# Kernel optimization log

Hardware: AMD Instinct MI355X
Metric: run time of the kernel (lower is better)

Reference implementation:

```python
import jax, jax.numpy as jnp
import numpy as np

N_NODES = 8192
N_EDGES = 65536
MUL = 16          # multiplicity of 0e and 1o irreps
NB = 16           # num_radial_basis
HID = 16          # num_radial_dimension
MAX_RADIUS = 5.0
SQRT3 = float(np.sqrt(3.0))


def soft_unit_step(x):
    # e3nn.math.soft_unit_step: exp(-1/x) for x>0 else 0 (grad-safe where)
    safe = jnp.where(x > 0, x, 1.0)
    return jnp.where(x > 0, jnp.exp(-1.0 / safe), 0.0)


def setup_inputs() -> dict:
    key = jax.random.key(0)
    ks = jax.random.split(key, 12)
    f_in = jax.random.normal(ks[0], (N_NODES, 4 * MUL), jnp.float32)
    edge_vec = jax.random.normal(ks[1], (N_EDGES, 3), jnp.float32) * 1.5
    edge_src = jax.random.randint(ks[2], (N_EDGES,), 0, N_NODES)
    edge_dst = jax.random.randint(ks[3], (N_EDGES,), 0, N_NODES)
    Wq0 = jax.random.normal(ks[4], (MUL, MUL), jnp.float32)
    Wq1 = jax.random.normal(ks[5], (MUL, MUL), jnp.float32)
    Wk1 = jax.random.normal(ks[6], (NB, HID), jnp.float32)
    Wk2 = jax.random.normal(ks[7], (HID, 4 * MUL * MUL), jnp.float32)
    Wv1 = jax.random.normal(ks[8], (NB, HID), jnp.float32)
    Wv2 = jax.random.normal(ks[9], (HID, 4 * MUL * MUL), jnp.float32)
    Wd0 = jax.random.normal(ks[10], (MUL, MUL), jnp.float32)
    Wd1 = jax.random.normal(ks[11], (MUL, MUL), jnp.float32)
    return dict(f_in=f_in, edge_vec=edge_vec, edge_src=edge_src, edge_dst=edge_dst,
                Wq0=Wq0, Wq1=Wq1, Wk1=Wk1, Wk2=Wk2, Wv1=Wv1, Wv2=Wv2, Wd0=Wd0, Wd1=Wd1)


def _forward(f_in, edge_vec, edge_src, edge_dst,
             Wq0, Wq1, Wk1, Wk2, Wv1, Wv2, Wd0, Wd1):
    f0 = f_in[:, :MUL]                         # [N, MUL]    0e scalars
    f1 = f_in[:, MUL:].reshape(-1, MUL, 3)     # [N, MUL, 3] 1o vectors

    r = jnp.linalg.norm(edge_vec, axis=1)      # [E]
    u = edge_vec / r[:, None]
    sh1 = SQRT3 * u                            # Y_1, component norm (|Y1|^2 = 3); Y_0 = 1

    # soft_one_hot_linspace, basis='smooth_finite', cutoff=True, * sqrt(NB)
    values = jnp.linspace(0.0, MAX_RADIUS, NB + 2)
    step = values[1] - values[0]
    diff = (r[:, None] - values[1:-1]) / step
    C = 1.14136 * float(np.exp(2.0))
    rb = (C * soft_unit_step(diff + 1.0) * soft_unit_step(1.0 - diff)) * np.sqrt(NB)

    edge_cut = soft_unit_step(10.0 * (1.0 - r / MAX_RADIUS))  # [E]

    def mlp(x, W1, W2):  # e3nn FullyConnectedNet with fan-in normalization
        h = jax.nn.silu(x @ (W1 / np.sqrt(NB)))
        return h @ (W2 / np.sqrt(HID))

    wk = mlp(rb, Wk1, Wk2).reshape(-1, 4, MUL, MUL)  # per-edge TP weights
    wv = mlp(rb, Wv1, Wv2).reshape(-1, 4, MUL, MUL)

    # h_q: per-irrep linear
    q0 = f0 @ Wq0 / np.sqrt(MUL)
    q1 = jnp.einsum('nic,io->noc', f1, Wq1) / np.sqrt(MUL)

    x0 = f0[edge_src]   # [E, MUL]
    x1 = f1[edge_src]   # [E, MUL, 3]

    def fctp(w):
        # FullyConnectedTensorProduct (16x0e+16x1o) x (0e+1o) -> (16x0e+16x1o)
        # 4 paths: 0x0->0, 1x1->0 (dot/sqrt3), 0x1->1, 1x0->1
        a = 1.0 / np.sqrt(2 * MUL)
        o0 = jnp.einsum('eij,ei->ej', w[:, 0], x0) \
           + jnp.einsum('eij,eic,ec->ej', w[:, 1], x1, sh1) / SQRT3
        o1 = jnp.einsum('eij,ei,ec->ejc', w[:, 2], x0, sh1) \
           + jnp.einsum('eij,eic->ejc', w[:, 3], x1)
        return o0 * a, o1 * a

    k0, k1 = fctp(wk)
    v0, v1 = fctp(wv)

    # dot_product: FCTP(query, key) -> 0e
    ad = 1.0 / np.sqrt(2.0 * MUL * MUL)
    dot = ad * (jnp.einsum('ij,ei,ej->e', Wd0, q0[edge_dst], k0)
                + jnp.einsum('ij,eic,ejc->e', Wd1, q1[edge_dst], k1) / SQRT3)

    exp = edge_cut * jnp.exp(dot)                                   # [E]
    z = jax.ops.segment_sum(exp, edge_dst, num_segments=N_NODES)    # [N]
    z = jnp.where(z == 0.0, 1.0, z)
    alpha = exp / z[edge_dst]
    # alpha.relu().sqrt() with grad-safe sqrt at 0
    s = jnp.where(alpha > 0, jnp.sqrt(jnp.where(alpha > 0, alpha, 1.0)), 0.0)

    f_out0 = jax.ops.segment_sum(s[:, None] * v0, edge_dst, num_segments=N_NODES)
    f_out1 = jax.ops.segment_sum(s[:, None, None] * v1, edge_dst, num_segments=N_NODES)
    return jnp.concatenate([f_out0, f_out1.reshape(-1, MUL * 3)], axis=-1)  # [N, 64]


def reference(f_in, edge_vec, edge_src, edge_dst,
              Wq0, Wq1, Wk1, Wk2, Wv1, Wv2, Wd0, Wd1):
    return _forward(f_in, edge_vec, edge_src, edge_dst,
                    Wq0, Wq1, Wk1, Wk2, Wv1, Wv2, Wd0, Wd1)
```

## Files before the change

### kernel.cpp

```cpp
#include <hip/hip_runtime.h>
#include <hip/hip_bf16.h>

#define N_NODES 8192
#define N_EDGES 65536

#define Z_OFF    0
#define CNT_OFF  8192
#define RP_OFF   16384
#define WF_OFF   24832
#define QD0_OFF  41216
#define QD1_OFF  172288
#define EXP_OFF  565504
#define EIDX_OFF 631040
#define V_OFF    696576

typedef _Float16 half8 __attribute__((ext_vector_type(8)));
typedef float f32x4 __attribute__((ext_vector_type(4)));

__device__ __forceinline__ float sus_f(float x) { return x > 0.f ? expf(-1.f / x) : 0.f; }
__device__ __forceinline__ float silu_f(float x) { return x / (1.f + expf(-x)); }

__device__ __forceinline__ half8 vmul(half8 v, _Float16 s) {
    half8 r;
#pragma unroll
    for (int d = 0; d < 8; ++d) r[d] = v[d] * s;
    return r;
}

__global__ __launch_bounds__(256) void k_prep(
    const float* __restrict__ f_in,
    const float* __restrict__ Wq0, const float* __restrict__ Wq1,
    const float* __restrict__ Wd0, const float* __restrict__ Wd1,
    const float* __restrict__ Wk2, const float* __restrict__ Wv2,
    const int* __restrict__ edst,
    half8* __restrict__ wfrag, float* __restrict__ qd0, float* __restrict__ qd1,
    int* __restrict__ cnt) {
    __shared__ float f0s[16][16];
    __shared__ float f1s[16][48];
    __shared__ float t0s[16][16];
    __shared__ float t1s[16][48];
    const int blk = blockIdx.x;
    const int tid = threadIdx.x;

    if (blk < 16) {
        int g = blk * 256 + tid;
        int lane = g & 63, t = (g >> 6) & 7, b = (g >> 9) & 3, kv = g >> 11;
        const float* src = kv ? Wv2 : Wk2;
        int n = lane & 15, quad = lane >> 4;
        const float SC = 0.044194173824159216f;
        half8 out;
#pragma unroll
        for (int d = 0; d < 8; ++d) {
            int k = t * 32 + quad * 8 + d;
            int i = k & 15, h = k >> 4;
            out[d] = (_Float16)(src[h * 1024 + b * 256 + i * 16 + n] * SC);
        }
        wfrag[g] = out;
        return;
    }
    if (blk >= 528) {
        int base = (blk - 528) * 256 + tid;
#pragma unroll
        for (int k = 0; k < 4; ++k) atomicAdd(cnt + edst[base + k * 16384], 1);
        return;
    }
    const int j = tid & 15, ln = tid >> 4;
    const int n = (blk - 16) * 16 + ln;
    f0s[ln][j]         = f_in[n * 64 + j];
    f1s[ln][j * 3 + 0] = f_in[n * 64 + 16 + j * 3 + 0];
    f1s[ln][j * 3 + 1] = f_in[n * 64 + 16 + j * 3 + 1];
    f1s[ln][j * 3 + 2] = f_in[n * 64 + 16 + j * 3 + 2];
    __syncthreads();
    float t0 = 0.f, ta = 0.f, tb = 0.f, tc = 0.f;
#pragma unroll
    for (int p = 0; p < 16; ++p) {
        float wq0 = Wq0[p * 16 + j];
        float wq1 = Wq1[p * 16 + j];
        t0 += f0s[ln][p] * wq0;
        ta += f1s[ln][p * 3 + 0] * wq1;
        tb += f1s[ln][p * 3 + 1] * wq1;
        tc += f1s[ln][p * 3 + 2] * wq1;
    }
    t0s[ln][j] = t0;
    t1s[ln][j * 3 + 0] = ta; t1s[ln][j * 3 + 1] = tb; t1s[ln][j * 3 + 2] = tc;
    __syncthreads();
    float q0a = 0.f, qa = 0.f, qb = 0.f, qc = 0.f;
#pragma unroll
    for (int i = 0; i < 16; ++i) {
        float wd0 = Wd0[i * 16 + j];
        float wd1 = Wd1[i * 16 + j];
        q0a += t0s[ln][i] * wd0;
        qa  += t1s[ln][i * 3 + 0] * wd1;
        qb  += t1s[ln][i * 3 + 1] * wd1;
        qc  += t1s[ln][i * 3 + 2] * wd1;
    }
    const float S0 = 0.011048543456f;
    const float S1 = 0.0063788674817f;
    qd0[n * 16 + j] = q0a * S0;
    qd1[0 * 131072 + n * 16 + j] = qa * S1;
    qd1[1 * 131072 + n * 16 + j] = qb * S1;
    qd1[2 * 131072 + n * 16 + j] = qc * S1;
}

__global__ __launch_bounds__(1024) void k_scan(int* __restrict__ cnt, int* __restrict__ rowptr) {
    __shared__ int part[1024];
    const int t = threadIdx.x;
    const int base = t * 8;
    int v[8]; int s = 0;
#pragma unroll
    for (int i = 0; i < 8; ++i) { v[i] = cnt[base + i]; s += v[i]; }
    part[t] = s;
    __syncthreads();
    for (int off = 1; off < 1024; off <<= 1) {
        int x = (t >= off) ? part[t - off] : 0;
        __syncthreads();
        part[t] += x;
        __syncthreads();
    }
    int run = part[t] - s;
#pragma unroll
    for (int i = 0; i < 8; ++i) { rowptr[base + i] = run; cnt[base + i] = run; run += v[i]; }
    if (t == 1023) rowptr[8192] = run;
}

__global__ void k_scidx(const int* __restrict__ edst, int* __restrict__ cnt,
                        int* __restrict__ eidx) {
    int e = blockIdx.x * blockDim.x + threadIdx.x;
    int slot = atomicAdd(cnt + edst[e], 1);
    eidx[slot] = e;
}

__global__ __launch_bounds__(256) void k_edge(
    const float* __restrict__ f_in, const float* __restrict__ evec,
    const int* __restrict__ esrc, const int* __restrict__ edst,
    const float* __restrict__ Wk1, const float* __restrict__ Wv1,
    const half8* __restrict__ wfrag,
    const float* __restrict__ qd0, const float* __restrict__ qd1,
    float* __restrict__ zbuf, float* __restrict__ expbuf, float* __restrict__ vbuf) {
    __shared__ __align__(16) _Float16 s_x0h[64][24];
    __shared__ __align__(16) _Float16 s_xsh[64][24];
    __shared__ __align__(16) _Float16 s_x1h[3][64][24];
    __shared__ __align__(16) _Float16 s_hkh[64][16];
    __shared__ __align__(16) _Float16 s_hvh[64][16];
    __shared__ float s_rb[64][16];
    __shared__ float s_sh[64][4];

    const int tid = threadIdx.x;
    const int e0 = blockIdx.x * 64;

    {
        const int el = tid >> 2, q = tid & 3;
        const int e = e0 + el;
        float v0 = evec[e * 3 + 0];
        float v1 = evec[e * 3 + 1];
        float v2 = evec[e * 3 + 2];
        float r = sqrtf(v0 * v0 + v1 * v1 + v2 * v2);
        float rs = r * 3.4f;
#pragma unroll
        for (int bb = 0; bb < 4; ++bb) {
            int b = q * 4 + bb;
            s_rb[el][b] = 33.734292f * sus_f(rs - (float)b) * sus_f((float)(b + 2) - rs);
        }
        if (q == 0) {
            float inv = r > 0.f ? 1.f / r : 0.f;
            const float SQ3 = 1.7320508075688772f;
            s_sh[el][0] = SQ3 * v0 * inv;
            s_sh[el][1] = SQ3 * v1 * inv;
            s_sh[el][2] = SQ3 * v2 * inv;
            s_sh[el][3] = sus_f(10.f - 2.f * r);
        }
    }
    __syncthreads();

    {
        const int j = tid & 15, slot = tid >> 4;
#pragma unroll
        for (int s = 0; s < 4; ++s) {
            const int el = slot * 4 + s;
            const int e = e0 + el;
            float aK = 0.f, aV = 0.f;
#pragma unroll
            for (int b = 0; b < 16; ++b) {
                float rbv = s_rb[el][b];
                aK += rbv * Wk1[b * 16 + j];
                aV += rbv * Wv1[b * 16 + j];
            }
            s_hkh[el][(j & 1) * 8 + (j >> 1)] = (_Float16)silu_f(aK * 0.25f);
            s_hvh[el][(j & 1) * 8 + (j >> 1)] = (_Float16)silu_f(aV * 0.25f);
            const int src = esrc[e];
            float x0 = f_in[src * 64 + j];
            float xa = f_in[src * 64 + 16 + j * 3 + 0];
            float xb = f_in[src * 64 + 16 + j * 3 + 1];
            float xc = f_in[src * 64 + 16 + j * 3 + 2];
            s_x0h[el][j] = (_Float16)x0;
            s_x1h[0][el][j] = (_Float16)xa;
            s_x1h[1][el][j] = (_Float16)xb;
            s_x1h[2][el][j] = (_Float16)xc;
            s_xsh[el][j] = (_Float16)((xa * s_sh[el][0] + xb * s_sh[el][1] + xc * s_sh[el][2])
                                      * 0.57735026919f);
        }
    }
    __syncthreads();

    const int lane = tid & 63;
    const int wv = tid >> 6;
    const int m = lane & 15, quad = lane >> 4;
    const int eb = wv * 16;
    const int eloc = eb + m;
    const int ihalf = quad >> 1;
    const int hh = (quad & 1) * 8;

    half8 X0 = *(const half8*)&s_x0h[eloc][hh];
    half8 XS = *(const half8*)&s_xsh[eloc][hh];
    half8 Xa = *(const half8*)&s_x1h[0][eloc][hh];
    half8 Xb = *(const half8*)&s_x1h[1][eloc][hh];
    half8 Xc = *(const half8*)&s_x1h[2][eloc][hh];
    half8 HK = *(const half8*)&s_hkh[eloc][ihalf * 8];
    half8 HV = *(const half8*)&s_hvh[eloc][ihalf * 8];

    {
        f32x4 o0 = {0.f, 0.f, 0.f, 0.f}, a1 = o0, ax = o0, ay = o0, az = o0;
#pragma unroll
        for (int t = 0; t < 8; ++t) {
            _Float16 hs = HK[t];
            half8 B0 = wfrag[(0 * 8 + t) * 64 + lane];
            half8 B1 = wfrag[(1 * 8 + t) * 64 + lane];
            half8 B2 = wfrag[(2 * 8 + t) * 64 + lane];
            half8 B3 = wfrag[(3 * 8 + t) * 64 + lane];
            half8 A0 = vmul(X0, hs);
            half8 As = vmul(XS, hs);
            half8 Aa = vmul(Xa, hs);
            half8 Ab = vmul(Xb, hs);
            half8 Ac = vmul(Xc, hs);
            o0 = __builtin_amdgcn_mfma_f32_16x16x32_f16(A0, B0, o0, 0, 0, 0);
            o0 = __builtin_amdgcn_mfma_f32_16x16x32_f16(As, B1, o0, 0, 0, 0);
            a1 = __builtin_amdgcn_mfma_f32_16x16x32_f16(A0, B2, a1, 0, 0, 0);
            ax = __builtin_amdgcn_mfma_f32_16x16x32_f16(Aa, B3, ax, 0, 0, 0);
            ay = __builtin_amdgcn_mfma_f32_16x16x32_f16(Ab, B3, ay, 0, 0, 0);
            az = __builtin_amdgcn_mfma_f32_16x16x32_f16(Ac, B3, az, 0, 0, 0);
        }
        const int j = m;
#pragma unroll
        for (int r = 0; r < 4; ++r) {
            const int el = eb + quad * 4 + r;
            const int e = e0 + el;
            const int dst = edst[e];
            float sh0 = s_sh[el][0], sh1 = s_sh[el][1], sh2 = s_sh[el][2];
            float k1x = a1[r] * sh0 + ax[r];
            float k1y = a1[r] * sh1 + ay[r];
            float k1z = a1[r] * sh2 + az[r];
            float dp = qd0[dst * 16 + j] * o0[r]
                     + qd1[0 * 131072 + dst * 16 + j] * k1x
                     + qd1[1 * 131072 + dst * 16 + j] * k1y
                     + qd1[2 * 131072 + dst * 16 + j] * k1z;
            dp += __shfl_xor(dp, 1);
            dp += __shfl_xor(dp, 2);
            dp += __shfl_xor(dp, 4);
            dp += __shfl_xor(dp, 8);
            if (j == 0) {
                float ev = s_sh[el][3] * expf(dp);
                expbuf[e] = ev;
                atomicAdd(zbuf + dst, ev);
            }
        }
    }

    {
        f32x4 o0 = {0.f, 0.f, 0.f, 0.f}, a1 = o0, ax = o0, ay = o0, az = o0;
        const half8* wfv = wfrag + 32 * 64;
#pragma unroll
        for (int t = 0; t < 8; ++t) {
            _Float16 hs = HV[t];
            half8 B0 = wfv[(0 * 8 + t) * 64 + lane];
            half8 B1 = wfv[(1 * 8 + t) * 64 + lane];
            half8 B2 = wfv[(2 * 8 + t) * 64 + lane];
            half8 B3 = wfv[(3 * 8 + t) * 64 + lane];
            half8 A0 = vmul(X0, hs);
            half8 As = vmul(XS, hs);
            half8 Aa = vmul(Xa, hs);
            half8 Ab = vmul(Xb, hs);
            half8 Ac = vmul(Xc, hs);
            o0 = __builtin_amdgcn_mfma_f32_16x16x32_f16(A0, B0, o0, 0, 0, 0);
            o0 = __builtin_amdgcn_mfma_f32_16x16x32_f16(As, B1, o0, 0, 0, 0);
            a1 = __builtin_amdgcn_mfma_f32_16x16x32_f16(A0, B2, a1, 0, 0, 0);
            ax = __builtin_amdgcn_mfma_f32_16x16x32_f16(Aa, B3, ax, 0, 0, 0);
            ay = __builtin_amdgcn_mfma_f32_16x16x32_f16(Ab, B3, ay, 0, 0, 0);
            az = __builtin_amdgcn_mfma_f32_16x16x32_f16(Ac, B3, az, 0, 0, 0);
        }
        const int j = m;
#pragma unroll
        for (int r = 0; r < 4; ++r) {
            const int el = eb + quad * 4 + r;
            const int e = e0 + el;
            float sh0 = s_sh[el][0], sh1 = s_sh[el][1], sh2 = s_sh[el][2];
            float* vp = vbuf + (size_t)e * 64;
            vp[j] = o0[r];
            vp[16 + j * 3 + 0] = a1[r] * sh0 + ax[r];
            vp[16 + j * 3 + 1] = a1[r] * sh1 + ay[r];
            vp[16 + j * 3 + 2] = a1[r] * sh2 + az[r];
        }
    }
}

__global__ __launch_bounds__(256) void k_out(
    const int* __restrict__ rowptr, const int* __restrict__ eidx,
    const float* __restrict__ expbuf, const float* __restrict__ zbuf,
    const float* __restrict__ vbuf, float* __restrict__ fout) {
    const int col = threadIdx.x & 63;
    const int n = blockIdx.x * 4 + (threadIdx.x >> 6);
    const int s0 = rowptr[n], s1 = rowptr[n + 1];
    float z = zbuf[n];
    float zinv = z > 0.f ? 1.f / z : 0.f;
    float acc = 0.f;
    for (int p = s0; p < s1; ++p) {
        int e = eidx[p];
        float ev = expbuf[e];
        float s = ev > 0.f ? sqrtf(ev * zinv) : 0.f;
        acc += s * vbuf[(size_t)e * 64 + col];
    }
    fout[n * 64 + col] = acc;
}

extern "C" void kernel_launch(void* const* d_in, const int* in_sizes, int n_in,
                              void* d_out, int out_size, void* d_ws, size_t ws_size,
                              hipStream_t stream) {
    const float* f_in = (const float*)d_in[0];
    const float* evec = (const float*)d_in[1];
    const int* esrc = (const int*)d_in[2];
    const int* edst = (const int*)d_in[3];
    const float* Wq0 = (const float*)d_in[4];
    const float* Wq1 = (const float*)d_in[5];
    const float* Wk1 = (const float*)d_in[6];
    const float* Wk2 = (const float*)d_in[7];
    const float* Wv1 = (const float*)d_in[8];
    const float* Wv2 = (const float*)d_in[9];
    const float* Wd0 = (const float*)d_in[10];
    const float* Wd1 = (const float*)d_in[11];

    float* ws    = (float*)d_ws;
    float* zbuf  = ws + Z_OFF;
    int*   cnt   = (int*)(ws + CNT_OFF);
    int*   rowptr= (int*)(ws + RP_OFF);
    half8* wfrag = (half8*)(ws + WF_OFF);
    float* qd0   = ws + QD0_OFF;
    float* qd1   = ws + QD1_OFF;
    float* expb  = ws + EXP_OFF;
    int*   eidx  = (int*)(ws + EIDX_OFF);
    float* vbuf  = ws + V_OFF;
    float* fout  = (float*)d_out;

    hipMemsetAsync(ws, 0, (size_t)16384 * sizeof(float), stream);

    k_prep<<<592, 256, 0, stream>>>(f_in, Wq0, Wq1, Wd0, Wd1, Wk2, Wv2, edst,
                                    wfrag, qd0, qd1, cnt);
    k_scan<<<1, 1024, 0, stream>>>(cnt, rowptr);
    k_scidx<<<N_EDGES / 256, 256, 0, stream>>>(edst, cnt, eidx);
    k_edge<<<N_EDGES / 64, 256, 0, stream>>>(f_in, evec, esrc, edst, Wk1, Wv1,
                                             wfrag, qd0, qd1, zbuf, expb, vbuf);
    k_out<<<N_NODES / 4, 256, 0, stream>>>(rowptr, eidx, expb, zbuf, vbuf, fout);
}
```

Measured before the change: 130.4 us.

## Scatter edge values into CSR order in edge kernel, store V as fp16

The edge kernel now claims a CSR slot per edge with an atomic cursor and writes exp and the value vector directly into destination-sorted order. This removes the separate scatter-index kernel, the z atomics and the indirect eidx gather in the output kernel. The softmax denominator is instead summed per node in the output kernel, and V is stored as fp16 through a shared-memory staging tile with vectorized 16-byte writes, halving its traffic. The scan is rewritten to use wave shuffles instead of a barrier-heavy shared-memory loop. The risks are reduced precision of V and a nondeterministic order of edges within each node.

New measurement: 127.1 us. -2.5%, faster.

```diff
diff --git a/kernel.cpp b/kernel.cpp
--- a/kernel.cpp
+++ b/kernel.cpp
@@ -4,15 +4,13 @@
 #define N_NODES 8192
 #define N_EDGES 65536
 
-#define Z_OFF    0
-#define CNT_OFF  8192
-#define RP_OFF   16384
-#define WF_OFF   24832
-#define QD0_OFF  41216
-#define QD1_OFF  172288
-#define EXP_OFF  565504
-#define EIDX_OFF 631040
-#define V_OFF    696576
+#define CNT_OFF  0
+#define RP_OFF   8192
+#define WF_OFF   16640
+#define QD0_OFF  33024
+#define QD1_OFF  164096
+#define EXP_OFF  557312
+#define VH_OFF   622848
 
 typedef _Float16 half8 __attribute__((ext_vector_type(8)));
 typedef float f32x4 __attribute__((ext_vector_type(4)));
@@ -103,31 +101,41 @@
 }
 
 __global__ __launch_bounds__(1024) void k_scan(int* __restrict__ cnt, int* __restrict__ rowptr) {
-    __shared__ int part[1024];
+    __shared__ int wsum[16];
+    __shared__ int woff[16];
     const int t = threadIdx.x;
+    const int lane = t & 63, wv = t >> 6;
     const int base = t * 8;
     int v[8]; int s = 0;
-#pragma unroll
-    for (int i = 0; i < 8; ++i) { v[i] = cnt[base + i]; s += v[i]; }
-    part[t] = s;
-    __syncthreads();
-    for (int off = 1; off < 1024; off <<= 1) {
-        int x = (t >= off) ? part[t - off] : 0;
-        __syncthreads();
-        part[t] += x;
-        __syncthreads();
-    }
-    int run = part[t] - s;
+    int4 p0 = ((const int4*)cnt)[t * 2];
+    int4 p1 = ((const int4*)cnt)[t * 2 + 1];
+    v[0] = p0.x; v[1] = p0.y; v[2] = p0.z; v[3] = p0.w;
+    v[4] = p1.x; v[5] = p1.y; v[6] = p1.z; v[7] = p1.w;
+#pragma unroll
+    for (int i = 0; i < 8; ++i) s += v[i];
+    int own = s;
+#pragma unroll
+    for (int off = 1; off < 64; off <<= 1) {
+        int u = __shfl_up(s, off);
+        if (lane >= off) s += u;
+    }
+    if (lane == 63) wsum[wv] = s;
+    __syncthreads();
+    if (wv == 0 && lane < 16) {
+        int u = wsum[lane];
+        int sc = u;
+#pragma unroll
+        for (int off = 1; off < 16; off <<= 1) {
+            int x = __shfl_up(sc, off);
+            if (lane >= off) sc += x;
+        }
+        woff[lane] = sc - u;
+    }
+    __syncthreads();
+    int run = woff[wv] + (s - own);
 #pragma unroll
     for (int i = 0; i < 8; ++i) { rowptr[base + i] = run; cnt[base + i] = run; run += v[i]; }
     if (t == 1023) rowptr[8192] = run;
-}
-
-__global__ void k_scidx(const int* __restrict__ edst, int* __restrict__ cnt,
-                        int* __restrict__ eidx) {
-    int e = blockIdx.x * blockDim.x + threadIdx.x;
-    int slot = atomicAdd(cnt + edst[e], 1);
-    eidx[slot] = e;
 }
 
 __global__ __launch_bounds__(256) void k_edge(
@@ -136,14 +144,16 @@
     const float* __restrict__ Wk1, const float* __restrict__ Wv1,
     const half8* __restrict__ wfrag,
     const float* __restrict__ qd0, const float* __restrict__ qd1,
-    float* __restrict__ zbuf, float* __restrict__ expbuf, float* __restrict__ vbuf) {
+    int* __restrict__ cursor, float* __restrict__ expbuf, _Float16* __restrict__ vh) {
     __shared__ __align__(16) _Float16 s_x0h[64][24];
     __shared__ __align__(16) _Float16 s_xsh[64][24];
     __shared__ __align__(16) _Float16 s_x1h[3][64][24];
     __shared__ __align__(16) _Float16 s_hkh[64][16];
     __shared__ __align__(16) _Float16 s_hvh[64][16];
+    __shared__ __align__(16) _Float16 s_vt[64][72];
     __shared__ float s_rb[64][16];
     __shared__ float s_sh[64][4];
+    __shared__ int   s_slot[64];
 
     const int tid = threadIdx.x;
     const int e0 = blockIdx.x * 64;
@@ -259,8 +269,9 @@
             dp += __shfl_xor(dp, 8);
             if (j == 0) {
                 float ev = s_sh[el][3] * expf(dp);
-                expbuf[e] = ev;
-                atomicAdd(zbuf + dst, ev);
+                int slot = atomicAdd(cursor + dst, 1);
+                s_slot[el] = slot;
+                expbuf[slot] = ev;
             }
         }
     }
@@ -291,32 +302,42 @@
 #pragma unroll
         for (int r = 0; r < 4; ++r) {
             const int el = eb + quad * 4 + r;
-            const int e = e0 + el;
             float sh0 = s_sh[el][0], sh1 = s_sh[el][1], sh2 = s_sh[el][2];
-            float* vp = vbuf + (size_t)e * 64;
-            vp[j] = o0[r];
-            vp[16 + j * 3 + 0] = a1[r] * sh0 + ax[r];
-            vp[16 + j * 3 + 1] = a1[r] * sh1 + ay[r];
-            vp[16 + j * 3 + 2] = a1[r] * sh2 + az[r];
-        }
+            s_vt[el][j] = (_Float16)o0[r];
+            s_vt[el][16 + j * 3 + 0] = (_Float16)(a1[r] * sh0 + ax[r]);
+            s_vt[el][16 + j * 3 + 1] = (_Float16)(a1[r] * sh1 + ay[r]);
+            s_vt[el][16 + j * 3 + 2] = (_Float16)(a1[r] * sh2 + az[r]);
+        }
+    }
+    __syncthreads();
+
+#pragma unroll
+    for (int pass = 0; pass < 2; ++pass) {
+        int row = pass * 32 + (tid >> 3);
+        int part = tid & 7;
+        half8 val = *(const half8*)&s_vt[row][part * 8];
+        int slot = s_slot[row];
+        *(half8*)(vh + (size_t)slot * 64 + part * 8) = val;
     }
 }
 
 __global__ __launch_bounds__(256) void k_out(
-    const int* __restrict__ rowptr, const int* __restrict__ eidx,
-    const float* __restrict__ expbuf, const float* __restrict__ zbuf,
-    const float* __restrict__ vbuf, float* __restrict__ fout) {
+    const int* __restrict__ rowptr,
+    const float* __restrict__ expbuf, const _Float16* __restrict__ vh,
+    float* __restrict__ fout) {
     const int col = threadIdx.x & 63;
     const int n = blockIdx.x * 4 + (threadIdx.x >> 6);
     const int s0 = rowptr[n], s1 = rowptr[n + 1];
-    float z = zbuf[n];
-    float zinv = z > 0.f ? 1.f / z : 0.f;
+    float zs = 0.f;
+    for (int p = s0 + col; p < s1; p += 64) zs += expbuf[p];
+#pragma unroll
+    for (int off = 32; off > 0; off >>= 1) zs += __shfl_xor(zs, off);
+    float zinv = zs > 0.f ? 1.f / zs : 0.f;
     float acc = 0.f;
     for (int p = s0; p < s1; ++p) {
-        int e = eidx[p];
-        float ev = expbuf[e];
+        float ev = expbuf[p];
         float s = ev > 0.f ? sqrtf(ev * zinv) : 0.f;
-        acc += s * vbuf[(size_t)e * 64 + col];
+        acc += s * (float)vh[(size_t)p * 64 + col];
     }
     fout[n * 64 + col] = acc;
 }
@@ -337,25 +358,22 @@
     const float* Wd0 = (const float*)d_in[10];
     const float* Wd1 = (const float*)d_in[11];
 
-    float* ws    = (float*)d_ws;
-    float* zbuf  = ws + Z_OFF;
-    int*   cnt   = (int*)(ws + CNT_OFF);
-    int*   rowptr= (int*)(ws + RP_OFF);
-    half8* wfrag = (half8*)(ws + WF_OFF);
-    float* qd0   = ws + QD0_OFF;
-    float* qd1   = ws + QD1_OFF;
-    float* expb  = ws + EXP_OFF;
-    int*   eidx  = (int*)(ws + EIDX_OFF);
-    float* vbuf  = ws + V_OFF;
-    float* fout  = (float*)d_out;
-
-    hipMemsetAsync(ws, 0, (size_t)16384 * sizeof(float), stream);
+    float* ws     = (float*)d_ws;
+    int*   cnt    = (int*)(ws + CNT_OFF);
+    int*   rowptr = (int*)(ws + RP_OFF);
+    half8* wfrag  = (half8*)(ws + WF_OFF);
+    float* qd0    = ws + QD0_OFF;
+    float* qd1    = ws + QD1_OFF;
+    float* expb   = ws + EXP_OFF;
+    _Float16* vh  = (_Float16*)(ws + VH_OFF);
+    float* fout   = (float*)d_out;
+
+    hipMemsetAsync(cnt, 0, (size_t)8192 * sizeof(int), stream);
 
     k_prep<<<592, 256, 0, stream>>>(f_in, Wq0, Wq1, Wd0, Wd1, Wk2, Wv2, edst,
                                     wfrag, qd0, qd1, cnt);
     k_scan<<<1, 1024, 0, stream>>>(cnt, rowptr);
-    k_scidx<<<N_EDGES / 256, 256, 0, stream>>>(edst, cnt, eidx);
     k_edge<<<N_EDGES / 64, 256, 0, stream>>>(f_in, evec, esrc, edst, Wk1, Wv1,
-                                             wfrag, qd0, qd1, zbuf, expb, vbuf);
-    k_out<<<N_NODES / 4, 256, 0, stream>>>(rowptr, eidx, expb, zbuf, vbuf, fout);
-}
+                                             wfrag, qd0, qd1, cnt, expb, vh);
+    k_out<<<N_NODES / 4, 256, 0, stream>>>(rowptr, expb, vh, fout);
+}
```
